# Kernel optimization log

Measured on AMD Instinct MI355X. Metric: run time of the kernel, lower is better.

## Reference

```python
import itertools
import jax, jax.numpy as jnp
import numpy as np

N_QUBITS = 8
N_LAYERS = 2
BATCH = 8192
INPUT_DIM = 3072
NUM_CLASSES = 10

_In = np.eye(2, dtype=np.complex64)
_Xn = np.array([[0, 1], [1, 0]], dtype=np.complex64)
_Yn = np.array([[0, -1j], [1j, 0]], dtype=np.complex64)
_Zn = np.array([[1, 0], [0, -1]], dtype=np.complex64)
_P = {"I": _In, "X": _Xn, "Y": _Yn, "Z": _Zn}
_XX = jnp.asarray(np.kron(_Xn, _Xn))
_YY = jnp.asarray(np.kron(_Yn, _Yn))
_ZZ = jnp.asarray(np.kron(_Zn, _Zn))
_I4 = jnp.eye(4, dtype=jnp.complex64)
# 2-qubit Pauli words in PennyLane ArbitraryUnitary order: IX, IY, IZ, XI, ..., ZZ
_WORDS = jnp.asarray(np.stack([np.kron(_P[a], _P[b]) for a, b in itertools.product("IXYZ", repeat=2)][1:]))


def apply_gate(state, U, wires):
    """Apply a 2^k x 2^k gate U to the given wires of a (2,)*n statevector."""
    n = state.ndim
    k = len(wires)
    U = U.reshape((2,) * (2 * k)).astype(state.dtype)
    state = jnp.tensordot(U, state, axes=(list(range(k, 2 * k)), list(wires)))
    rest = [a for a in range(n) if a not in wires]
    perm = [0] * n
    for i, a in enumerate(wires):
        perm[a] = i
    for j, a in enumerate(rest):
        perm[a] = k + j
    return jnp.transpose(state, perm)


def u3_mat(t, p, d):
    ct, st = jnp.cos(t / 2).astype(jnp.complex64), jnp.sin(t / 2).astype(jnp.complex64)
    r0 = jnp.stack([ct, -jnp.exp(1j * d) * st])
    r1 = jnp.stack([jnp.exp(1j * p) * st, jnp.exp(1j * (p + d)) * ct])
    return jnp.stack([r0, r1])


def ry_mat(t):
    c, s = jnp.cos(t / 2), jnp.sin(t / 2)
    return jnp.stack([jnp.stack([c, -s]), jnp.stack([s, c])]).astype(jnp.complex64)


def ising_mat(phi, pauli2):
    # exp(-i phi/2 P) for two-qubit Pauli word P (P^2 = I)
    return jnp.cos(phi / 2) * _I4 - 1j * jnp.sin(phi / 2) * pauli2


def circuit(conv_w, pool_w, last_w, feats):
    state = jnp.zeros((2,) * N_QUBITS, jnp.complex64).at[(0,) * N_QUBITS].set(1.0)
    # AngleEmbedding with RY rotations
    for w in range(N_QUBITS):
        state = apply_gate(state, ry_mat(feats[w]), (w,))
    wires = list(range(N_QUBITS))
    for layer in range(N_LAYERS):
        cw = conv_w[layer]
        nw = len(wires)
        for p in (0, 1):
            for idx in range(nw - 1):
                if idx % 2 == p:
                    a, b = wires[idx], wires[idx + 1]
                    state = apply_gate(state, u3_mat(cw[idx, 0], cw[idx, 1], cw[idx, 2]), (a,))
                    state = apply_gate(state, u3_mat(cw[idx + 1, 3], cw[idx + 1, 4], cw[idx + 1, 5]), (b,))
                    state = apply_gate(state, ising_mat(cw[idx, 6], _ZZ), (a, b))
                    state = apply_gate(state, ising_mat(cw[idx, 7], _YY), (a, b))
                    state = apply_gate(state, ising_mat(cw[idx, 8], _XX), (a, b))
                    state = apply_gate(state, u3_mat(cw[idx, 9], cw[idx, 10], cw[idx, 11]), (a,))
                    state = apply_gate(state, u3_mat(cw[idx + 1, 12], cw[idx + 1, 13], cw[idx + 1, 14]), (b,))
        # Pooling: mid-circuit measure + conditional U3 == (deferred measurement)
        pw = pool_w[layer]
        for idx in range(1, nw, 2):
            u = u3_mat(pw[idx // 2, 0], pw[idx // 2, 1], pw[idx // 2, 2])
            cu = jnp.zeros((4, 4), jnp.complex64).at[0, 0].set(1.0).at[1, 1].set(1.0).at[2:, 2:].set(u)
            state = apply_gate(state, cu, (wires[idx], wires[idx - 1]))
        wires = wires[::2]
    # ArbitraryUnitary on remaining 2 wires: product of 15 PauliRot gates
    for k in range(15):
        mat = jnp.cos(last_w[k] / 2) * _I4 - 1j * jnp.sin(last_w[k] / 2) * _WORDS[k]
        state = apply_gate(state, mat, tuple(wires))
    probs = state.real ** 2 + state.imag ** 2
    z = jnp.sum(probs, axis=tuple(range(1, N_QUBITS)))  # (2,)
    return z[0] - z[1]


def setup_inputs() -> dict:
    key = jax.random.key(0)
    ks = jax.random.split(key, 8)
    return {
        "x": jax.random.normal(ks[0], (BATCH, INPUT_DIM), jnp.float32),
        "fc_w": jax.random.normal(ks[1], (N_QUBITS, INPUT_DIM), jnp.float32) * 0.02,
        "fc_b": jnp.zeros((N_QUBITS,), jnp.float32),
        "conv_params": jax.random.normal(ks[2], (N_LAYERS, N_QUBITS, 15), jnp.float32),
        "pool_params": jax.random.normal(ks[3], (N_LAYERS, N_QUBITS // 2, 3), jnp.float32),
        "last_params": jax.random.normal(ks[4], (15,), jnp.float32),
        "out_w": jax.random.normal(ks[5], (NUM_CLASSES, 1), jnp.float32),
        "out_b": jnp.zeros((NUM_CLASSES,), jnp.float32),
    }


def reference(x, fc_w, fc_b, conv_params, pool_params, last_params, out_w, out_b):
    feats = jnp.tanh(x.reshape(x.shape[0], -1) @ fc_w.T + fc_b)  # (B, n_qubits)
    qvals = jax.vmap(lambda f: circuit(conv_params, pool_params, last_params, f))(feats)
    logits = qvals[:, None].astype(x.dtype) @ out_w.T + out_b  # (B, num_classes)
    return logits
```

## Files before the change

kernel.cpp:

```cpp
#include <hip/hip_runtime.h>
#include <math.h>

__constant__ int G_ORD[17] = {0,1,2,3,4,5,6, 10,11,12,13, 7,8,9, 14,15, 16};
__constant__ int G_WA[17]  = {0,2,4,6,1,3,5, 1,3,5,7, 0,4,2, 2,6, 0};
__constant__ int G_WB[17]  = {1,3,5,7,2,4,6, 0,2,4,6, 2,6,4, 0,4, 4};
__constant__ int CDESC[10][3] = {{0,0,1},{0,2,3},{0,4,5},{0,6,7},{0,1,2},{0,3,4},{0,5,6},
                                 {1,0,1},{1,2,3},{1,1,2}};
__constant__ int PDESC[6][2] = {{0,0},{0,1},{0,2},{0,3},{1,0},{1,1}};
__constant__ float2 PMAT[4][4] = {
  {{1.f,0.f},{0.f,0.f},{0.f,0.f},{1.f,0.f}},
  {{0.f,0.f},{1.f,0.f},{1.f,0.f},{0.f,0.f}},
  {{0.f,0.f},{0.f,-1.f},{0.f,1.f},{0.f,0.f}},
  {{1.f,0.f},{0.f,0.f},{0.f,0.f},{-1.f,0.f}}};

__device__ __forceinline__ float2 cmul(float2 a, float2 b){
  return make_float2(a.x*b.x - a.y*b.y, a.x*b.y + a.y*b.x);
}
__device__ __forceinline__ float2 cadd(float2 a, float2 b){
  return make_float2(a.x+b.x, a.y+b.y);
}

__device__ void u3m(float t, float p, float d, float2* u){
  float ct = cosf(0.5f*t), st = sinf(0.5f*t);
  u[0] = make_float2(ct, 0.f);
  u[1] = make_float2(-cosf(d)*st, -sinf(d)*st);
  u[2] = make_float2(cosf(p)*st,  sinf(p)*st);
  u[3] = make_float2(cosf(p+d)*ct, sinf(p+d)*ct);
}

__global__ __launch_bounds__(320) void build_u_kernel(
    const float* __restrict__ conv, const float* __restrict__ pool,
    const float* __restrict__ last, float2* __restrict__ U){
  __shared__ float2 gm[2][17][16];
  __shared__ float2 gl[17][16];
  __shared__ float2 st[256];
  int t = threadIdx.x, col = blockIdx.x;
  {
    int g = t >> 4, e = t & 15, r = e >> 2, c = e & 3;
    float2 A1[4], B1[4], A2[4], B2[4];
    int nsteps = 0;
    if (g < 10){
      int layer = CDESC[g][0], ra = CDESC[g][1], rb = CDESC[g][2];
      const float* cw = conv + layer*120;
      int bA = ra*15, bB = rb*15;
      u3m(cw[bA+0],  cw[bA+1],  cw[bA+2],  A1);
      u3m(cw[bB+3],  cw[bB+4],  cw[bB+5],  B1);
      u3m(cw[bA+9],  cw[bA+10], cw[bA+11], A2);
      u3m(cw[bB+12], cw[bB+13], cw[bB+14], B2);
      nsteps = 5;
    } else if (g < 16){
      nsteps = 1;
    } else if (g == 16){
      nsteps = 16;
    }
    for (int s = 0; s < 16; s++){
      if (g < 17 && s < nsteps){
        float2 T = make_float2(0.f, 0.f);
        if (g < 10){
          if (s == 0){
            T = cmul(A1[(r>>1)*2 + (c>>1)], B1[(r&1)*2 + (c&1)]);
          } else if (s <= 3){
            int layer = CDESC[g][0], ra = CDESC[g][1];
            float phi = conv[layer*120 + ra*15 + 5 + s];
            int q_ = 4 - s;
            float ch = cosf(0.5f*phi), sh = sinf(0.5f*phi);
            #pragma unroll
            for (int k=0;k<4;k++){
              float2 w = cmul(PMAT[q_][(r>>1)*2 + (k>>1)], PMAT[q_][(r&1)*2 + (k&1)]);
              float2 rk = make_float2(sh*w.y, -sh*w.x);
              if (k == r) rk.x += ch;
              T = cadd(T, cmul(rk, gm[s&1][g][k*4 + c]));
            }
          } else {
            #pragma unroll
            for (int k=0;k<4;k++){
              float2 k2 = cmul(A2[(r>>1)*2 + (k>>1)], B2[(r&1)*2 + (k&1)]);
              T = cadd(T, cmul(k2, gm[s&1][g][k*4 + c]));
            }
          }
        } else if (g < 16){
          int layer = PDESC[g-10][0], h = PDESC[g-10][1];
          const float* pw = pool + layer*12 + h*3;
          float2 u[4];
          u3m(pw[0], pw[1], pw[2], u);
          if (e == 0 || e == 5) T = make_float2(1.f, 0.f);
          else if (e == 10) T = u[0];
          else if (e == 11) T = u[1];
          else if (e == 14) T = u[2];
          else if (e == 15) T = u[3];
        } else {
          if (s == 0){
            T = make_float2((r==c)?1.f:0.f, 0.f);
          } else {
            int w_ = s;
            int qa = w_ >> 2, qb = w_ & 3;
            float phi = last[s-1];
            float ch = cosf(0.5f*phi), sh = sinf(0.5f*phi);
            #pragma unroll
            for (int k=0;k<4;k++){
              float2 w = cmul(PMAT[qa][(r>>1)*2 + (k>>1)], PMAT[qb][(r&1)*2 + (k&1)]);
              float2 rk = make_float2(sh*w.y, -sh*w.x);
              if (k == r) rk.x += ch;
              T = cadd(T, cmul(rk, gm[s&1][16][k*4 + c]));
            }
          }
        }
        gm[(s+1)&1][g][e] = T;
        if (s == nsteps-1) gl[g][e] = T;
      }
      __syncthreads();
    }
  }
  if (t < 256) st[t] = make_float2(t==col ? 1.f : 0.f, 0.f);
  __syncthreads();
  for (int g=0; g<17; g++){
    if (t < 64){
      int slot = G_ORD[g];
      float2 m[16];
      #pragma unroll
      for (int i=0;i<16;i++) m[i] = gl[slot][i];
      int pa = 7 - G_WA[g], pb = 7 - G_WB[g];
      int plo = pa < pb ? pa : pb, phi_ = pa < pb ? pb : pa;
      int mm = t;
      int t1   = ((mm >> plo) << (plo+1)) | (mm & ((1<<plo)-1));
      int base = ((t1 >> phi_) << (phi_+1)) | (t1 & ((1<<phi_)-1));
      int ba = 1<<pa, bb = 1<<pb;
      int i0 = base, i1 = base|bb, i2 = base|ba, i3 = base|ba|bb;
      float2 s0 = st[i0], s1 = st[i1], s2 = st[i2], s3 = st[i3];
      float2 n0 = cadd(cadd(cmul(m[0], s0), cmul(m[1], s1)), cadd(cmul(m[2], s2), cmul(m[3], s3)));
      float2 n1 = cadd(cadd(cmul(m[4], s0), cmul(m[5], s1)), cadd(cmul(m[6], s2), cmul(m[7], s3)));
      float2 n2 = cadd(cadd(cmul(m[8], s0), cmul(m[9], s1)), cadd(cmul(m[10],s2), cmul(m[11],s3)));
      float2 n3 = cadd(cadd(cmul(m[12],s0), cmul(m[13],s1)), cadd(cmul(m[14],s2), cmul(m[15],s3)));
      st[i0] = n0; st[i1] = n1; st[i2] = n2; st[i3] = n3;
    }
    __syncthreads();
  }
  if (t < 256) U[t*256 + col] = st[t];
}

__global__ __launch_bounds__(256) void build_a_kernel(
    const float2* __restrict__ U, float* __restrict__ A){
  int j = threadIdx.x, i = blockIdx.x;
  float a = 0.f;
  #pragma unroll 8
  for (int k=0; k<256; k++){
    float2 uj = U[k*256 + j];
    float2 ui = U[k*256 + i];
    float sgn = (k < 128) ? 1.f : -1.f;
    a += sgn*(ui.x*uj.x + ui.y*uj.y);
  }
  A[i*256 + j] = a;
}

__global__ __launch_bounds__(256, 4) void main_kernel(
    const float* __restrict__ x, const float* __restrict__ fcw,
    const float* __restrict__ fcb, const float* __restrict__ Ag,
    const float* __restrict__ outw, const float* __restrict__ outb,
    float* __restrict__ out){
  __shared__ float lds[6528];
  float* ps    = lds;
  float* flds  = lds + 2048;
  float* pqred = lds + 2112;
  float* red   = lds + 2176;
  int t = threadIdx.x, lane = t & 63, wv = t >> 6, jb = lane;
  int r0 = blockIdx.x * 8;
  {
    int rw = r0 + wv*2;
    const float4* x4 = (const float4*)x;
    const float4* w4 = (const float4*)fcw;
    float acc[2][8];
    #pragma unroll
    for (int r=0;r<2;r++)
      #pragma unroll
      for (int o=0;o<8;o++) acc[r][o] = 0.f;
    #pragma unroll 2
    for (int p=0; p<12; p++){
      float4 wf[8];
      #pragma unroll
      for (int o=0;o<8;o++) wf[o] = w4[o*768 + p*64 + lane];
      #pragma unroll
      for (int r=0;r<2;r++){
        float4 xv = x4[(size_t)(rw+r)*768 + p*64 + lane];
        #pragma unroll
        for (int o=0;o<8;o++){
          acc[r][o] += xv.x*wf[o].x + xv.y*wf[o].y + xv.z*wf[o].z + xv.w*wf[o].w;
        }
      }
    }
    #pragma unroll
    for (int r=0;r<2;r++)
      #pragma unroll
      for (int o=0;o<8;o++)
        red[((wv*2+r)*8 + o)*68 + lane] = acc[r][o];
  }
  __syncthreads();
  if (t < 64){
    const float4* rp = (const float4*)(red + t*68);
    float4 s4 = make_float4(0.f,0.f,0.f,0.f);
    #pragma unroll
    for (int i=0;i<16;i++){
      float4 v = rp[i];
      s4.x += v.x; s4.y += v.y; s4.z += v.z; s4.w += v.w;
    }
    flds[t] = tanhf(s4.x + s4.y + s4.z + s4.w + fcb[t & 7]);
  }
  __syncthreads();
  if (t < 128){
    int row = t >> 4, i1 = t & 15;
    float fv[8];
    #pragma unroll
    for (int w=0; w<8; w++) fv[w] = flds[row*8 + w];
    float cc[8], ss[8];
    #pragma unroll
    for (int w=0; w<8; w++){
      float a = 0.5f*fv[w];
      __sincosf(a, &ss[w], &cc[w]);
    }
    float Hv = (i1&8 ? ss[0]:cc[0]) * (i1&4 ? ss[1]:cc[1])
             * (i1&2 ? ss[2]:cc[2]) * (i1&1 ? ss[3]:cc[3]);
    float l2[2], l4[4], l8[8], L[16];
    l2[0]=cc[4]; l2[1]=ss[4];
    #pragma unroll
    for (int a=0;a<2;a++){ l4[a*2]=l2[a]*cc[5]; l4[a*2+1]=l2[a]*ss[5]; }
    #pragma unroll
    for (int a=0;a<4;a++){ l8[a*2]=l4[a]*cc[6]; l8[a*2+1]=l4[a]*ss[6]; }
    #pragma unroll
    for (int a=0;a<8;a++){ L[a*2]=l8[a]*cc[7]; L[a*2+1]=l8[a]*ss[7]; }
    float4* dst = (float4*)(ps + row*256 + i1*16);
    #pragma unroll
    for (int qd=0; qd<4; qd++)
      dst[qd] = make_float4(Hv*L[qd*4+0], Hv*L[qd*4+1],
                            Hv*L[qd*4+2], Hv*L[qd*4+3]);
  }
  __syncthreads();
  const float4* ps4 = (const float4*)ps;
  const float4* Ag4 = (const float4*)Ag;
  float4 acc4[8];
  #pragma unroll
  for (int r=0;r<8;r++) acc4[r] = make_float4(0.f,0.f,0.f,0.f);
  int kbase = wv*16;
  #pragma unroll 2
  for (int kq=0; kq<16; kq++){
    int grp = kbase + kq;
    float4 av0 = Ag4[(grp*4+0)*64 + jb];
    float4 av1 = Ag4[(grp*4+1)*64 + jb];
    float4 av2 = Ag4[(grp*4+2)*64 + jb];
    float4 av3 = Ag4[(grp*4+3)*64 + jb];
    #pragma unroll
    for (int r=0; r<8; r++){
      float4 pv = ps4[r*64 + grp];
      acc4[r].x += pv.x*av0.x + pv.y*av1.x + pv.z*av2.x + pv.w*av3.x;
      acc4[r].y += pv.x*av0.y + pv.y*av1.y + pv.z*av2.y + pv.w*av3.y;
      acc4[r].z += pv.x*av0.z + pv.y*av1.z + pv.z*av2.z + pv.w*av3.z;
      acc4[r].w += pv.x*av0.w + pv.y*av1.w + pv.z*av2.w + pv.w*av3.w;
    }
  }
  float p[8];
  #pragma unroll
  for (int r=0; r<8; r++){
    float4 psv = ps4[r*64 + jb];
    float pr = acc4[r].x*psv.x + acc4[r].y*psv.y + acc4[r].z*psv.z + acc4[r].w*psv.w;
    #pragma unroll
    for (int m=1; m<64; m<<=1) pr += __shfl_xor(pr, m, 64);
    p[r] = pr;
  }
  if (jb == 0){
    #pragma unroll
    for (int r=0; r<8; r++) pqred[wv*8 + r] = p[r];
  }
  __syncthreads();
  if (t < 80){
    int row = t / 10, c = t - row*10;
    float q = (pqred[row] + pqred[8 + row]) + (pqred[16 + row] + pqred[24 + row]);
    out[(r0 + row)*10 + c] = q*outw[c] + outb[c];
  }
}

extern "C" void kernel_launch(void* const* d_in, const int* in_sizes, int n_in,
                              void* d_out, int out_size, void* d_ws, size_t ws_size,
                              hipStream_t stream) {
  const float* x    = (const float*)d_in[0];
  const float* fcw  = (const float*)d_in[1];
  const float* fcb  = (const float*)d_in[2];
  const float* conv = (const float*)d_in[3];
  const float* pool = (const float*)d_in[4];
  const float* last = (const float*)d_in[5];
  const float* outw = (const float*)d_in[6];
  const float* outb = (const float*)d_in[7];
  float* out = (float*)d_out;

  float* ws = (float*)d_ws;
  float2* U  = (float2*)ws;
  float*  Am = ws + 131072;

  build_u_kernel<<<256, 320, 0, stream>>>(conv, pool, last, U);
  build_a_kernel<<<256, 256, 0, stream>>>(U, Am);
  main_kernel<<<1024, 256, 0, stream>>>(x, fcw, fcb, Am, outw, outb, out);
}
```

Baseline: 248.2 us.

## Process 16 rows per block and stage fc weights through double-buffered LDS

Each block now handles 16 batch rows instead of 8, so every fetch of the fc weights and of the 256x256 A matrix serves twice as many rows. The fc weights are staged through a double-buffered shared-memory tile with a software prefetch of the next chunk, instead of each wave reading them directly from global memory. This cuts global and L2 traffic for weights and A, at the cost of more registers (16 accumulator vectors, launch bounds lowered to 2), a larger LDS footprint, half as many blocks, and a barrier on every k-chunk.

Result: no change. 247.0 us (median of 2 runs) (-0.5%).

```diff
diff --git a/kernel.cpp b/kernel.cpp
--- a/kernel.cpp
+++ b/kernel.cpp
@@ -152,49 +152,67 @@
   A[i*256 + j] = a;
 }
 
-__global__ __launch_bounds__(256, 4) void main_kernel(
+__global__ __launch_bounds__(256, 2) void main_kernel(
     const float* __restrict__ x, const float* __restrict__ fcw,
     const float* __restrict__ fcb, const float* __restrict__ Ag,
     const float* __restrict__ outw, const float* __restrict__ outb,
     float* __restrict__ out){
-  __shared__ float lds[6528];
+  __shared__ float lds[12992];
+  float* red   = lds;
   float* ps    = lds;
-  float* flds  = lds + 2048;
-  float* pqred = lds + 2112;
-  float* red   = lds + 2176;
+  float4* wb4  = (float4*)(lds + 8704);
+  float* flds  = lds + 12800;
+  float* pqred = lds + 12928;
   int t = threadIdx.x, lane = t & 63, wv = t >> 6, jb = lane;
-  int r0 = blockIdx.x * 8;
+  int r0 = blockIdx.x * 16;
   {
-    int rw = r0 + wv*2;
+    int rw = r0 + wv*4;
     const float4* x4 = (const float4*)x;
     const float4* w4 = (const float4*)fcw;
-    float acc[2][8];
-    #pragma unroll
-    for (int r=0;r<2;r++)
+    float acc[4][8];
+    #pragma unroll
+    for (int r=0;r<4;r++)
       #pragma unroll
       for (int o=0;o<8;o++) acc[r][o] = 0.f;
-    #pragma unroll 2
+    {
+      int i0 = t, i1 = t + 256;
+      wb4[i0] = w4[(i0>>6)*768 + (i0&63)];
+      wb4[i1] = w4[(i1>>6)*768 + (i1&63)];
+    }
+    __syncthreads();
     for (int p=0; p<12; p++){
+      int cb = p & 1, nb = cb ^ 1;
+      float4 sg0, sg1;
+      if (p < 11){
+        int i0 = t, i1 = t + 256;
+        sg0 = w4[(i0>>6)*768 + (p+1)*64 + (i0&63)];
+        sg1 = w4[(i1>>6)*768 + (p+1)*64 + (i1&63)];
+      }
       float4 wf[8];
       #pragma unroll
-      for (int o=0;o<8;o++) wf[o] = w4[o*768 + p*64 + lane];
-      #pragma unroll
-      for (int r=0;r<2;r++){
+      for (int o=0;o<8;o++) wf[o] = wb4[cb*512 + o*64 + lane];
+      #pragma unroll
+      for (int r=0;r<4;r++){
         float4 xv = x4[(size_t)(rw+r)*768 + p*64 + lane];
         #pragma unroll
         for (int o=0;o<8;o++){
           acc[r][o] += xv.x*wf[o].x + xv.y*wf[o].y + xv.z*wf[o].z + xv.w*wf[o].w;
         }
       }
-    }
-    #pragma unroll
-    for (int r=0;r<2;r++)
+      if (p < 11){
+        wb4[nb*512 + t]       = sg0;
+        wb4[nb*512 + t + 256] = sg1;
+      }
+      __syncthreads();
+    }
+    #pragma unroll
+    for (int r=0;r<4;r++)
       #pragma unroll
       for (int o=0;o<8;o++)
-        red[((wv*2+r)*8 + o)*68 + lane] = acc[r][o];
-  }
-  __syncthreads();
-  if (t < 64){
+        red[((wv*4+r)*8 + o)*68 + lane] = acc[r][o];
+  }
+  __syncthreads();
+  if (t < 128){
     const float4* rp = (const float4*)(red + t*68);
     float4 s4 = make_float4(0.f,0.f,0.f,0.f);
     #pragma unroll
@@ -205,7 +223,7 @@
     flds[t] = tanhf(s4.x + s4.y + s4.z + s4.w + fcb[t & 7]);
   }
   __syncthreads();
-  if (t < 128){
+  {
     int row = t >> 4, i1 = t & 15;
     float fv[8];
     #pragma unroll
@@ -235,9 +253,9 @@
   __syncthreads();
   const float4* ps4 = (const float4*)ps;
   const float4* Ag4 = (const float4*)Ag;
-  float4 acc4[8];
+  float4 acc4[16];
   #pragma unroll
-  for (int r=0;r<8;r++) acc4[r] = make_float4(0.f,0.f,0.f,0.f);
+  for (int r=0;r<16;r++) acc4[r] = make_float4(0.f,0.f,0.f,0.f);
   int kbase = wv*16;
   #pragma unroll 2
   for (int kq=0; kq<16; kq++){
@@ -247,7 +265,7 @@
     float4 av2 = Ag4[(grp*4+2)*64 + jb];
     float4 av3 = Ag4[(grp*4+3)*64 + jb];
     #pragma unroll
-    for (int r=0; r<8; r++){
+    for (int r=0; r<16; r++){
       float4 pv = ps4[r*64 + grp];
       acc4[r].x += pv.x*av0.x + pv.y*av1.x + pv.z*av2.x + pv.w*av3.x;
       acc4[r].y += pv.x*av0.y + pv.y*av1.y + pv.z*av2.y + pv.w*av3.y;
@@ -255,23 +273,18 @@
       acc4[r].w += pv.x*av0.w + pv.y*av1.w + pv.z*av2.w + pv.w*av3.w;
     }
   }
-  float p[8];
   #pragma unroll
-  for (int r=0; r<8; r++){
+  for (int r=0; r<16; r++){
     float4 psv = ps4[r*64 + jb];
     float pr = acc4[r].x*psv.x + acc4[r].y*psv.y + acc4[r].z*psv.z + acc4[r].w*psv.w;
     #pragma unroll
     for (int m=1; m<64; m<<=1) pr += __shfl_xor(pr, m, 64);
-    p[r] = pr;
-  }
-  if (jb == 0){
-    #pragma unroll
-    for (int r=0; r<8; r++) pqred[wv*8 + r] = p[r];
-  }
-  __syncthreads();
-  if (t < 80){
+    if (jb == 0) pqred[wv*16 + r] = pr;
+  }
+  __syncthreads();
+  if (t < 160){
     int row = t / 10, c = t - row*10;
-    float q = (pqred[row] + pqred[8 + row]) + (pqred[16 + row] + pqred[24 + row]);
+    float q = (pqred[row] + pqred[16 + row]) + (pqred[32 + row] + pqred[48 + row]);
     out[(r0 + row)*10 + c] = q*outw[c] + outb[c];
   }
 }
@@ -295,5 +308,5 @@
 
   build_u_kernel<<<256, 320, 0, stream>>>(conv, pool, last, U);
   build_a_kernel<<<256, 256, 0, stream>>>(U, Am);
-  main_kernel<<<1024, 256, 0, stream>>>(x, fcw, fcb, Am, outw, outb, out);
-}
+  main_kernel<<<512, 256, 0, stream>>>(x, fcw, fcb, Am, outw, outb, out);
+}
```

## Split fused kernel into feature and quadratic-form kernels with 16-row tiles

Applied to the files above, without the earlier changes.

Splits the single main kernel into a feature kernel, which writes the 256-entry product-state vectors to workspace, and a quadratic-form kernel that processes 16 rows per block instead of 8. Doubling the rows per block halves the number of reads of the 256x256 A matrix per row. The feature kernel also double-buffers the x and fc_w loads across the 12 reduction steps to overlap memory latency with compute. The cost is an extra launch, an 8 MB round-trip through global memory for the intermediate vectors, and higher register pressure from 16 accumulators.

Measured after the change: 388.4 us. 1.57x slower.

```diff
diff --git a/kernel.cpp b/kernel.cpp
--- a/kernel.cpp
+++ b/kernel.cpp
@@ -152,17 +152,12 @@
   A[i*256 + j] = a;
 }
 
-__global__ __launch_bounds__(256, 4) void main_kernel(
+__global__ __launch_bounds__(256, 4) void feats_kernel(
     const float* __restrict__ x, const float* __restrict__ fcw,
-    const float* __restrict__ fcb, const float* __restrict__ Ag,
-    const float* __restrict__ outw, const float* __restrict__ outb,
-    float* __restrict__ out){
-  __shared__ float lds[6528];
-  float* ps    = lds;
-  float* flds  = lds + 2048;
-  float* pqred = lds + 2112;
-  float* red   = lds + 2176;
-  int t = threadIdx.x, lane = t & 63, wv = t >> 6, jb = lane;
+    const float* __restrict__ fcb, float* __restrict__ psig){
+  __shared__ float red[4352];
+  __shared__ float flds[64];
+  int t = threadIdx.x, lane = t & 63, wv = t >> 6;
   int r0 = blockIdx.x * 8;
   {
     int rw = r0 + wv*2;
@@ -173,17 +168,27 @@
     for (int r=0;r<2;r++)
       #pragma unroll
       for (int o=0;o<8;o++) acc[r][o] = 0.f;
-    #pragma unroll 2
+    float4 wfb[2][8], xvb[2][2];
+    #pragma unroll
+    for (int o=0;o<8;o++) wfb[0][o] = w4[o*768 + lane];
+    #pragma unroll
+    for (int r=0;r<2;r++) xvb[0][r] = x4[(size_t)(rw+r)*768 + lane];
+    #pragma unroll
     for (int p=0; p<12; p++){
-      float4 wf[8];
-      #pragma unroll
-      for (int o=0;o<8;o++) wf[o] = w4[o*768 + p*64 + lane];
+      const int cb = p & 1, nb = cb ^ 1;
+      if (p < 11){
+        #pragma unroll
+        for (int o=0;o<8;o++) wfb[nb][o] = w4[o*768 + (p+1)*64 + lane];
+        #pragma unroll
+        for (int r=0;r<2;r++) xvb[nb][r] = x4[(size_t)(rw+r)*768 + (p+1)*64 + lane];
+      }
       #pragma unroll
       for (int r=0;r<2;r++){
-        float4 xv = x4[(size_t)(rw+r)*768 + p*64 + lane];
+        float4 xv = xvb[cb][r];
         #pragma unroll
         for (int o=0;o<8;o++){
-          acc[r][o] += xv.x*wf[o].x + xv.y*wf[o].y + xv.z*wf[o].z + xv.w*wf[o].w;
+          float4 wf = wfb[cb][o];
+          acc[r][o] += xv.x*wf.x + xv.y*wf.y + xv.z*wf.z + xv.w*wf.w;
         }
       }
     }
@@ -226,18 +231,34 @@
     for (int a=0;a<4;a++){ l8[a*2]=l4[a]*cc[6]; l8[a*2+1]=l4[a]*ss[6]; }
     #pragma unroll
     for (int a=0;a<8;a++){ L[a*2]=l8[a]*cc[7]; L[a*2+1]=l8[a]*ss[7]; }
-    float4* dst = (float4*)(ps + row*256 + i1*16);
+    float4* dst = (float4*)(psig + (size_t)(r0+row)*256 + i1*16);
     #pragma unroll
     for (int qd=0; qd<4; qd++)
       dst[qd] = make_float4(Hv*L[qd*4+0], Hv*L[qd*4+1],
                             Hv*L[qd*4+2], Hv*L[qd*4+3]);
   }
+}
+
+__global__ __launch_bounds__(256, 4) void quad_kernel(
+    const float* __restrict__ psig, const float* __restrict__ Ag,
+    const float* __restrict__ outw, const float* __restrict__ outb,
+    float* __restrict__ out){
+  __shared__ float ps[4096];
+  __shared__ float pqred[64];
+  int t = threadIdx.x, jb = t & 63, wv = t >> 6;
+  int r0 = blockIdx.x * 16;
+  {
+    float4* psl4 = (float4*)ps;
+    const float4* pg4 = (const float4*)psig;
+    #pragma unroll
+    for (int i=t; i<1024; i+=256) psl4[i] = pg4[(size_t)r0*64 + i];
+  }
   __syncthreads();
   const float4* ps4 = (const float4*)ps;
   const float4* Ag4 = (const float4*)Ag;
-  float4 acc4[8];
+  float4 acc4[16];
   #pragma unroll
-  for (int r=0;r<8;r++) acc4[r] = make_float4(0.f,0.f,0.f,0.f);
+  for (int r=0;r<16;r++) acc4[r] = make_float4(0.f,0.f,0.f,0.f);
   int kbase = wv*16;
   #pragma unroll 2
   for (int kq=0; kq<16; kq++){
@@ -247,7 +268,7 @@
     float4 av2 = Ag4[(grp*4+2)*64 + jb];
     float4 av3 = Ag4[(grp*4+3)*64 + jb];
     #pragma unroll
-    for (int r=0; r<8; r++){
+    for (int r=0; r<16; r++){
       float4 pv = ps4[r*64 + grp];
       acc4[r].x += pv.x*av0.x + pv.y*av1.x + pv.z*av2.x + pv.w*av3.x;
       acc4[r].y += pv.x*av0.y + pv.y*av1.y + pv.z*av2.y + pv.w*av3.y;
@@ -255,23 +276,18 @@
       acc4[r].w += pv.x*av0.w + pv.y*av1.w + pv.z*av2.w + pv.w*av3.w;
     }
   }
-  float p[8];
   #pragma unroll
-  for (int r=0; r<8; r++){
+  for (int r=0; r<16; r++){
     float4 psv = ps4[r*64 + jb];
     float pr = acc4[r].x*psv.x + acc4[r].y*psv.y + acc4[r].z*psv.z + acc4[r].w*psv.w;
     #pragma unroll
     for (int m=1; m<64; m<<=1) pr += __shfl_xor(pr, m, 64);
-    p[r] = pr;
-  }
-  if (jb == 0){
-    #pragma unroll
-    for (int r=0; r<8; r++) pqred[wv*8 + r] = p[r];
-  }
-  __syncthreads();
-  if (t < 80){
+    if (jb == 0) pqred[wv*16 + r] = pr;
+  }
+  __syncthreads();
+  if (t < 160){
     int row = t / 10, c = t - row*10;
-    float q = (pqred[row] + pqred[8 + row]) + (pqred[16 + row] + pqred[24 + row]);
+    float q = (pqred[row] + pqred[16 + row]) + (pqred[32 + row] + pqred[48 + row]);
     out[(r0 + row)*10 + c] = q*outw[c] + outb[c];
   }
 }
@@ -290,10 +306,12 @@
   float* out = (float*)d_out;
 
   float* ws = (float*)d_ws;
-  float2* U  = (float2*)ws;
-  float*  Am = ws + 131072;
+  float2* U    = (float2*)ws;
+  float*  Am   = ws + 131072;
+  float*  psig = ws + 196608;
 
   build_u_kernel<<<256, 320, 0, stream>>>(conv, pool, last, U);
   build_a_kernel<<<256, 256, 0, stream>>>(U, Am);
-  main_kernel<<<1024, 256, 0, stream>>>(x, fcw, fcb, Am, outw, outb, out);
-}
+  feats_kernel<<<1024, 256, 0, stream>>>(x, fcw, fcb, psig);
+  quad_kernel<<<512, 256, 0, stream>>>(psig, Am, outw, outb, out);
+}
```

## Double-buffer x and fc_w tiles into LDS via async global_load_lds

Applied to the files above, without the earlier changes.

The feature projection stage now stages x rows and fc_w chunks into a double-buffered LDS region using global_load_lds, prefetching the next chunk while computing on the current one. Previously each wave loaded all 8 weight rows directly from global memory every iteration, redundantly across waves. LDS use grows and launch bounds drop to 2 blocks per SM, so occupancy falls, and each iteration adds a full vmcnt wait plus a barrier.

Result: slower. 256.1 us (+3.2%).

```diff
diff --git a/kernel.cpp b/kernel.cpp
--- a/kernel.cpp
+++ b/kernel.cpp
@@ -26,6 +26,12 @@
   u[1] = make_float2(-cosf(d)*st, -sinf(d)*st);
   u[2] = make_float2(cosf(p)*st,  sinf(p)*st);
   u[3] = make_float2(cosf(p+d)*ct, sinf(p+d)*ct);
+}
+
+__device__ __forceinline__ void stage16(const float4* g, float4* l){
+  __builtin_amdgcn_global_load_lds(
+      (const __attribute__((address_space(1))) void*)g,
+      (__attribute__((address_space(3))) void*)l, 16, 0, 0);
 }
 
 __global__ __launch_bounds__(320) void build_u_kernel(
@@ -152,40 +158,59 @@
   A[i*256 + j] = a;
 }
 
-__global__ __launch_bounds__(256, 4) void main_kernel(
+__global__ __launch_bounds__(256, 2) void main_kernel(
     const float* __restrict__ x, const float* __restrict__ fcw,
     const float* __restrict__ fcb, const float* __restrict__ Ag,
     const float* __restrict__ outw, const float* __restrict__ outb,
     float* __restrict__ out){
-  __shared__ float lds[6528];
+  __shared__ float lds[12640];
+  float4* xt   = (float4*)lds;
+  float* red   = lds + 8192;
+  float* flds  = lds + 12544;
+  float* pqred = lds + 12608;
   float* ps    = lds;
-  float* flds  = lds + 2048;
-  float* pqred = lds + 2112;
-  float* red   = lds + 2176;
   int t = threadIdx.x, lane = t & 63, wv = t >> 6, jb = lane;
   int r0 = blockIdx.x * 8;
+  const float4* x4 = (const float4*)x;
+  const float4* w4 = (const float4*)fcw;
   {
-    int rw = r0 + wv*2;
-    const float4* x4 = (const float4*)x;
-    const float4* w4 = (const float4*)fcw;
     float acc[2][8];
     #pragma unroll
     for (int r=0;r<2;r++)
       #pragma unroll
       for (int o=0;o<8;o++) acc[r][o] = 0.f;
-    #pragma unroll 2
+    #pragma unroll
+    for (int r=0;r<2;r++)
+      stage16(x4 + (size_t)(r0+wv*2+r)*768 + lane, xt + (wv*2+r)*64);
+    #pragma unroll
+    for (int o=0;o<2;o++)
+      stage16(w4 + (size_t)(wv*2+o)*768 + lane, xt + 512 + (wv*2+o)*64);
+    asm volatile("s_waitcnt vmcnt(0)" ::: "memory");
+    __syncthreads();
     for (int p=0; p<12; p++){
+      const int cb = p & 1, nb = cb ^ 1;
+      if (p < 11){
+        #pragma unroll
+        for (int r=0;r<2;r++)
+          stage16(x4 + (size_t)(r0+wv*2+r)*768 + (p+1)*64 + lane,
+                  xt + nb*1024 + (wv*2+r)*64);
+        #pragma unroll
+        for (int o=0;o<2;o++)
+          stage16(w4 + (size_t)(wv*2+o)*768 + (p+1)*64 + lane,
+                  xt + nb*1024 + 512 + (wv*2+o)*64);
+      }
       float4 wf[8];
       #pragma unroll
-      for (int o=0;o<8;o++) wf[o] = w4[o*768 + p*64 + lane];
+      for (int o=0;o<8;o++) wf[o] = xt[cb*1024 + 512 + o*64 + lane];
       #pragma unroll
       for (int r=0;r<2;r++){
-        float4 xv = x4[(size_t)(rw+r)*768 + p*64 + lane];
+        float4 xv = xt[cb*1024 + (wv*2+r)*64 + lane];
         #pragma unroll
-        for (int o=0;o<8;o++){
+        for (int o=0;o<8;o++)
           acc[r][o] += xv.x*wf[o].x + xv.y*wf[o].y + xv.z*wf[o].z + xv.w*wf[o].w;
-        }
       }
+      asm volatile("s_waitcnt vmcnt(0)" ::: "memory");
+      __syncthreads();
     }
     #pragma unroll
     for (int r=0;r<2;r++)
@@ -255,18 +280,18 @@
       acc4[r].w += pv.x*av0.w + pv.y*av1.w + pv.z*av2.w + pv.w*av3.w;
     }
   }
-  float p[8];
+  float p2[8];
   #pragma unroll
   for (int r=0; r<8; r++){
     float4 psv = ps4[r*64 + jb];
     float pr = acc4[r].x*psv.x + acc4[r].y*psv.y + acc4[r].z*psv.z + acc4[r].w*psv.w;
     #pragma unroll
     for (int m=1; m<64; m<<=1) pr += __shfl_xor(pr, m, 64);
-    p[r] = pr;
+    p2[r] = pr;
   }
   if (jb == 0){
     #pragma unroll
-    for (int r=0; r<8; r++) pqred[wv*8 + r] = p[r];
+    for (int r=0; r<8; r++) pqred[wv*8 + r] = p2[r];
   }
   __syncthreads();
   if (t < 80){
```
